# Kernel optimization log

Hardware: AMD Instinct MI355X
Metric: run time of the kernel (lower is better)

Reference implementation:

```python
import jax, jax.numpy as jnp
import numpy as np

HEADS = 4


def rel_to_abs(x):
    """Convert relative logits [..., L, 2L-1] to absolute [..., L, L].
    out[..., i, j] = x[..., i, j - i + L - 1]."""
    L = x.shape[-2]
    idx = jnp.arange(L)[None, :] - jnp.arange(L)[:, None] + (L - 1)  # [L, L]
    idx = jnp.broadcast_to(idx, x.shape[:-1] + (L,))
    return jnp.take_along_axis(x, idx, axis=-1)


def setup_inputs() -> dict:
    key = jax.random.key(0)
    ks = jax.random.split(key, 5)
    b, c, h, w = 2, 256, 64, 64
    dh = c // HEADS
    return {
        "x": jax.random.normal(ks[0], (b, c, h, w), jnp.float32),
        "w_qkv": jax.random.normal(ks[1], (3 * c, c), jnp.float32) / np.float32(np.sqrt(c)),
        "w_out": jax.random.normal(ks[2], (c, c), jnp.float32) / np.float32(np.sqrt(c)),
        "rel_height": jax.random.normal(ks[3], (2 * h - 1, dh), jnp.float32),
        "rel_width": jax.random.normal(ks[4], (2 * w - 1, dh), jnp.float32),
    }


def reference(x, w_qkv, w_out, rel_height, rel_width):
    b, c, h, w = x.shape
    dh = c // HEADS
    N = h * w
    scale = dh ** -0.5

    # 1x1 conv == per-pixel matmul over channels
    qkv = jnp.einsum('bchw,oc->bohw', x, w_qkv)  # [b, 3c, h, w]
    q, k, v = jnp.split(qkv, 3, axis=1)

    def to_heads(t):  # [b, c, h, w] -> [b, H, N, dh]
        return t.reshape(b, HEADS, dh, N).transpose(0, 1, 3, 2)

    q = to_heads(q) * scale
    k = to_heads(k)
    v = to_heads(v)

    # content-content scores over spatial positions
    content = jnp.einsum('bnid,bnjd->bnij', q, k)  # [b, H, N, N]

    q5 = q.reshape(b, HEADS, h, w, dh)  # [b, H, x, y, dh]
    # width relative logits: [b,H,x,y,2w-1] -> abs -> [b,H,x,y,jw]
    rw = rel_to_abs(jnp.einsum('bnxyd,rd->bnxyr', q5, rel_width))
    # height relative logits on transposed spatial: [b,H,y,x,2h-1] -> [b,H,y,x,jh]
    rh = rel_to_abs(jnp.einsum('bnyxd,rd->bnyxr', q5.transpose(0, 1, 3, 2, 4), rel_height))

    logits = content.reshape(b, HEADS, h, w, h, w)
    logits = logits + rw[:, :, :, :, None, :]  # broadcast width bias over target height jh
    logits = logits + rh.transpose(0, 1, 3, 2, 4)[:, :, :, :, :, None]  # [b,H,x,y,jh] over jw

    attn = jax.nn.softmax(logits.reshape(b, HEADS, N, N), axis=-1)
    out = jnp.einsum('bnij,bnjd->bnid', attn, v)  # [b, H, N, dh]
    out = out.transpose(0, 1, 3, 2).reshape(b, c, h, w)
    out = jnp.einsum('bchw,oc->bohw', out, w_out)  # 1x1 out projection
    return out + x
```

## Files before the change

kernel.cpp:

```cpp
#include <hip/hip_runtime.h>

typedef unsigned short u16;
typedef unsigned int u32;
typedef __bf16 bf16x8 __attribute__((ext_vector_type(8)));
typedef __bf16 bf16x2 __attribute__((ext_vector_type(2)));
typedef float f32x4 __attribute__((ext_vector_type(4)));
typedef float f32x2 __attribute__((ext_vector_type(2)));
typedef u32 u32x4 __attribute__((ext_vector_type(4)));
typedef u32 u32x2 __attribute__((ext_vector_type(2)));
typedef short s16x4 __attribute__((ext_vector_type(4)));

#define DEVI __device__ __forceinline__

#if defined(__has_builtin)
#if __has_builtin(__builtin_amdgcn_exp2f)
#define EXP2F(x) __builtin_amdgcn_exp2f(x)
#endif
#endif
#ifndef EXP2F
#define EXP2F(x) exp2f(x)
#endif

#define MFMA16(a, b, c) __builtin_amdgcn_mfma_f32_16x16x32_bf16(a, b, c, 0, 0, 0)
#define MFMA1K(a, b, c) __builtin_amdgcn_mfma_f32_16x16x16bf16_1k(a, b, c, 0, 0, 0)

DEVI u16 f2bf(float f) {
    u32 u = __builtin_bit_cast(u32, f);
    u = (u + 0x7FFFu + ((u >> 16) & 1u)) >> 16;
    return (u16)u;
}
DEVI float bf2f(u16 h) {
    u32 u = ((u32)h) << 16;
    return __builtin_bit_cast(float, u);
}
DEVI float bfhi(u32 u) { return __builtin_bit_cast(float, u & 0xFFFF0000u); }
DEVI float bflo(u32 u) { return __builtin_bit_cast(float, u << 16); }
DEVI bf16x8 bc8(u32x4 u) { return __builtin_bit_cast(bf16x8, u); }
DEVI u32 pack2(float a, float b) {
    f32x2 v = {a, b};
    bf16x2 h = __builtin_convertvector(v, bf16x2);
    return __builtin_bit_cast(u32, h);
}

#define QSCALE 0.18033688011112042f

__global__ __launch_bounds__(256) void k_prep(const float* __restrict__ x,
                                              const float* __restrict__ wq,
                                              const float* __restrict__ wo,
                                              const float* __restrict__ relh,
                                              const float* __restrict__ relw,
                                              u16* __restrict__ xt, u16* __restrict__ wqb,
                                              u16* __restrict__ wob, u16* __restrict__ relhb,
                                              u16* __restrict__ relwb) {
    int bid = blockIdx.x;
    int t = threadIdx.x;
    if (bid < 512) {
        int pm = bid & 63, cm = (bid >> 6) & 3, b = bid >> 8;
        int p0 = pm * 64, c0 = cm * 64;
        __shared__ float tile[64][65];
#pragma unroll
        for (int it = 0; it < 16; ++it) {
            int idx = it * 256 + t;
            int cl = idx >> 6, pl = idx & 63;
            tile[cl][pl] = x[((size_t)(b * 256 + c0 + cl)) * 4096 + p0 + pl];
        }
        __syncthreads();
#pragma unroll
        for (int it = 0; it < 16; ++it) {
            int idx = it * 256 + t;
            int pl = idx >> 6, cl = idx & 63;
            xt[((size_t)(b * 4096 + p0 + pl)) * 256 + c0 + cl] = f2bf(tile[cl][pl]);
        }
    } else {
        int i0 = (bid - 512) * 256 + t;
#pragma unroll
        for (int i = i0; i < 196608; i += 65536) wqb[i] = f2bf(wq[i]);
        if (i0 < 65536) wob[i0] = f2bf(wo[i0]);
        if (i0 < 8192) {
            relhb[i0] = (i0 < 8128) ? f2bf(relh[i0]) : (u16)0;
            relwb[i0] = (i0 < 8128) ? f2bf(relw[i0]) : (u16)0;
        }
    }
}

__global__ __launch_bounds__(256) void k_qkv(const u16* __restrict__ xt, const u16* __restrict__ wqb,
                                             const u16* __restrict__ relwb,
                                             const u16* __restrict__ relhb,
                                             u16* __restrict__ q, u16* __restrict__ k,
                                             u16* __restrict__ vt, u16* __restrict__ Wabs,
                                             u16* __restrict__ Habs) {
    int pm = blockIdx.x, on = blockIdx.y, b = blockIdx.z;
    int p0 = pm * 64, o0 = on * 64;
    __shared__ __align__(16) u16 Bt[64 * 264];
    int t = threadIdx.x;
    int wv = t >> 6, l = t & 63, quad = l >> 4, li = l & 15;

    u32x4 areg[8];
    const u32x4* arow = (const u32x4*)(xt + ((size_t)(b * 4096 + p0 + wv * 16 + li)) * 256);
#pragma unroll
    for (int kc = 0; kc < 8; ++kc) areg[kc] = arow[kc * 4 + quad];

    {
        int row = t >> 2, c0 = (t & 3) * 64;
        const u32x4* g = (const u32x4*)(wqb + (size_t)(o0 + row) * 256 + c0);
        u32x4* s = (u32x4*)(Bt + row * 264 + c0);
#pragma unroll
        for (int kk = 0; kk < 8; ++kk) s[kk] = g[kk];
    }
    __syncthreads();

    f32x4 acc[4] = {{0, 0, 0, 0}, {0, 0, 0, 0}, {0, 0, 0, 0}, {0, 0, 0, 0}};
#pragma unroll
    for (int kc = 0; kc < 8; ++kc) {
        bf16x8 a = bc8(areg[kc]);
#pragma unroll
        for (int ct = 0; ct < 4; ++ct) {
            bf16x8 bb = bc8(*(const u32x4*)(Bt + (ct * 16 + li) * 264 + kc * 32 + quad * 8));
            acc[ct] = MFMA16(a, bb, acc[ct]);
        }
    }

    int tensor = on >> 2, head = on & 3;
    if (tensor == 2) {
        __syncthreads();
        u16* T = Bt;
#pragma unroll
        for (int ct = 0; ct < 4; ++ct)
#pragma unroll
            for (int r = 0; r < 4; ++r)
                T[(ct * 16 + li) * 72 + wv * 16 + quad * 4 + r] = f2bf(acc[ct][r]);
        __syncthreads();
        int dr = t >> 2, pc = (t & 3) * 16;
        u32x4* g = (u32x4*)(vt + ((size_t)((b * 4 + head) * 64 + dr)) * 4096 + p0 + pc);
        const u32x4* s2 = (const u32x4*)(T + dr * 72 + pc);
        g[0] = s2[0];
        g[1] = s2[1];
    } else {
        u16* outp = (tensor == 0) ? q : k;
        float sc = (tensor == 0) ? QSCALE : 1.0f;
#pragma unroll
        for (int ct = 0; ct < 4; ++ct)
#pragma unroll
            for (int r = 0; r < 4; ++r) {
                int p = p0 + wv * 16 + quad * 4 + r;
                int d = ct * 16 + li;
                outp[((size_t)((b * 4 + head) * 4096 + p)) * 64 + d] = f2bf(acc[ct][r] * sc);
            }
        if (tensor == 0) {
            int bh = b * 4 + head;
            u16* T = Bt;
            u16* Ls = Bt + 64 * 72;
            __syncthreads();
#pragma unroll
            for (int ct = 0; ct < 4; ++ct)
#pragma unroll
                for (int r = 0; r < 4; ++r)
                    T[(wv * 16 + quad * 4 + r) * 72 + ct * 16 + li] = f2bf(acc[ct][r] * QSCALE);
            {
                int row = t >> 1, half = t & 1;
                const u32x4* g2 = (const u32x4*)(relwb + row * 64 + half * 32);
                u32x4* s2 = (u32x4*)(Ls + row * 72 + half * 32);
#pragma unroll
                for (int kk = 0; kk < 4; ++kk) s2[kk] = g2[kk];
            }
            __syncthreads();
            u32x4 aq2[2];
            aq2[0] = *(const u32x4*)(T + (wv * 16 + li) * 72 + quad * 8);
            aq2[1] = *(const u32x4*)(T + (wv * 16 + li) * 72 + 32 + quad * 8);

            f32x4 acc2[8];
#pragma unroll
            for (int ct = 0; ct < 8; ++ct) acc2[ct] = (f32x4){0.f, 0.f, 0.f, 0.f};
#pragma unroll
            for (int kc = 0; kc < 2; ++kc) {
                bf16x8 a = bc8(aq2[kc]);
#pragma unroll
                for (int ct = 0; ct < 8; ++ct) {
                    bf16x8 bb = bc8(*(const u32x4*)(Ls + (ct * 16 + li) * 72 + kc * 32 + quad * 8));
                    acc2[ct] = MFMA16(a, bb, acc2[ct]);
                }
            }
#pragma unroll
            for (int ct = 0; ct < 8; ++ct)
#pragma unroll
                for (int r = 0; r < 4; ++r) {
                    int row = wv * 16 + quad * 4 + r;
                    int j = (ct * 16 + li) - 63 + row;
                    if (j >= 0 && j < 64)
                        Wabs[((size_t)(bh * 4096 + p0 + row)) * 64 + j] = f2bf(acc2[ct][r]);
                }
            __syncthreads();
            {
                int row = t >> 1, half = t & 1;
                const u32x4* g2 = (const u32x4*)(relhb + row * 64 + half * 32);
                u32x4* s2 = (u32x4*)(Ls + row * 72 + half * 32);
#pragma unroll
                for (int kk = 0; kk < 4; ++kk) s2[kk] = g2[kk];
            }
            __syncthreads();
#pragma unroll
            for (int ct = 0; ct < 8; ++ct) acc2[ct] = (f32x4){0.f, 0.f, 0.f, 0.f};
#pragma unroll
            for (int kc = 0; kc < 2; ++kc) {
                bf16x8 a = bc8(aq2[kc]);
#pragma unroll
                for (int ct = 0; ct < 8; ++ct) {
                    bf16x8 bb = bc8(*(const u32x4*)(Ls + (ct * 16 + li) * 72 + kc * 32 + quad * 8));
                    acc2[ct] = MFMA16(a, bb, acc2[ct]);
                }
            }
#pragma unroll
            for (int ct = 0; ct < 8; ++ct)
#pragma unroll
                for (int r = 0; r < 4; ++r) {
                    int row = wv * 16 + quad * 4 + r;
                    int j = (ct * 16 + li) - 63 + pm;
                    if (j >= 0 && j < 64)
                        Habs[((size_t)(bh * 4096 + p0 + row)) * 64 + j] = f2bf(acc2[ct][r]);
                }
        }
    }
}

__global__ __launch_bounds__(256, 2) void k_flash(const u16* __restrict__ q,
                                                  const u16* __restrict__ kg,
                                                  const u16* __restrict__ vt,
                                                  const u16* __restrict__ Wabs,
                                                  const u16* __restrict__ Habs,
                                                  u16* __restrict__ OP,
                                                  float* __restrict__ LS) {
    int pm = blockIdx.x, bh = blockIdx.y, ks = blockIdx.z;
    int p0 = pm * 128;
    __shared__ __align__(16) u16 Kt[2][64 * 72];
    __shared__ __align__(16) u16 Vl[2][64 * 72];
    __shared__ __align__(16) u16 Hl[128 * 24];
    int t = threadIdx.x, wv = t >> 6, l = t & 63, quad = l >> 4, li = l & 15;
    int rbase = wv * 32;

    u32x4 aq[2][2];
#pragma unroll
    for (int rs = 0; rs < 2; ++rs) {
        const u32x4* qrow =
            (const u32x4*)(q + ((size_t)(bh * 4096 + p0 + rbase + rs * 16 + li)) * 64);
        aq[rs][0] = qrow[quad];
        aq[rs][1] = qrow[4 + quad];
    }

    f32x4 wb4[2][4];
#pragma unroll
    for (int rs = 0; rs < 2; ++rs)
#pragma unroll
        for (int ct = 0; ct < 4; ++ct) {
            const u32* wp = (const u32*)(Wabs +
                                         ((size_t)(bh * 4096 + p0 + rbase + rs * 16 + li)) * 64 +
                                         ct * 16 + quad * 4);
            u32 lo = wp[0], hi = wp[1];
            wb4[rs][ct] = (f32x4){bflo(lo), bfhi(lo), bflo(hi), bfhi(hi)};
        }

    {
        int row = t >> 1, half = t & 1;
        const u32x4* g =
            (const u32x4*)(Habs + ((size_t)(bh * 4096 + p0 + row)) * 64 + ks * 16 + half * 8);
        *(u32x4*)(Hl + row * 24 + half * 8) = g[0];
    }

    int srow = t >> 2, scc = (t & 3) * 16;
    {
        int j0 = ks * 1024;
        const u32x4* gk = (const u32x4*)(kg + ((size_t)(bh * 4096 + j0 + srow)) * 64 + scc);
        u32x4* sk = (u32x4*)(Kt[0] + srow * 72 + scc);
        sk[0] = gk[0];
        sk[1] = gk[1];
        const u32x4* gv = (const u32x4*)(vt + ((size_t)(bh * 64 + srow)) * 4096 + j0 + scc);
        u32x4* sv = (u32x4*)(Vl[0] + srow * 72 + scc);
        sv[0] = gv[0];
        sv[1] = gv[1];
    }

    f32x4 oacc[2][5];
#pragma unroll
    for (int rs = 0; rs < 2; ++rs)
#pragma unroll
        for (int ct = 0; ct < 5; ++ct) oacc[rs][ct] = (f32x4){0.f, 0.f, 0.f, 0.f};

    const s16x4 ones = {(short)0x3F80, (short)0x3F80, (short)0x3F80, (short)0x3F80};

    u32x4 kreg[2], vreg[2];
    for (int kt = 0; kt < 16; ++kt) {
        __syncthreads();
        int cur = kt & 1;
        const u16* Kc = Kt[cur];
        const u16* Vc = Vl[cur];
        if (kt < 15) {
            int j0 = (ks * 16 + kt + 1) * 64;
            const u32x4* gk = (const u32x4*)(kg + ((size_t)(bh * 4096 + j0 + srow)) * 64 + scc);
            kreg[0] = gk[0];
            kreg[1] = gk[1];
            const u32x4* gv = (const u32x4*)(vt + ((size_t)(bh * 64 + srow)) * 4096 + j0 + scc);
            vreg[0] = gv[0];
            vreg[1] = gv[1];
        }

        float hh0 = bf2f(Hl[(rbase + li) * 24 + kt]);
        float hh1 = bf2f(Hl[(rbase + 16 + li) * 24 + kt]);
        f32x4 s[2][4];
#pragma unroll
        for (int ct = 0; ct < 4; ++ct) {
            s[0][ct] = wb4[0][ct] + hh0;
            s[1][ct] = wb4[1][ct] + hh1;
        }
#pragma unroll
        for (int kc = 0; kc < 2; ++kc) {
            bf16x8 b0 = bc8(aq[0][kc]), b1 = bc8(aq[1][kc]);
#pragma unroll
            for (int ct = 0; ct < 4; ++ct) {
                bf16x8 af = bc8(*(const u32x4*)(Kc + (ct * 16 + li) * 72 + kc * 32 + quad * 8));
                s[0][ct] = MFMA16(af, b0, s[0][ct]);
                s[1][ct] = MFMA16(af, b1, s[1][ct]);
            }
        }

        s16x4 pf[2][4];
#pragma unroll
        for (int rs = 0; rs < 2; ++rs)
#pragma unroll
            for (int ct = 0; ct < 4; ++ct) {
                u32x2 pp;
                pp.x = pack2(EXP2F(s[rs][ct][0]), EXP2F(s[rs][ct][1]));
                pp.y = pack2(EXP2F(s[rs][ct][2]), EXP2F(s[rs][ct][3]));
                pf[rs][ct] = __builtin_bit_cast(s16x4, pp);
            }

#pragma unroll
        for (int jt = 0; jt < 4; ++jt) {
            s16x4 a0 = pf[0][jt], a1 = pf[1][jt];
#pragma unroll
            for (int dt = 0; dt < 4; ++dt) {
                s16x4 bv = __builtin_bit_cast(
                    s16x4, *(const u32x2*)(Vc + (dt * 16 + li) * 72 + jt * 16 + quad * 4));
                oacc[0][dt] = MFMA1K(a0, bv, oacc[0][dt]);
                oacc[1][dt] = MFMA1K(a1, bv, oacc[1][dt]);
            }
            oacc[0][4] = MFMA1K(a0, ones, oacc[0][4]);
            oacc[1][4] = MFMA1K(a1, ones, oacc[1][4]);
        }

        if (kt < 15) {
            u32x4* sk = (u32x4*)(Kt[cur ^ 1] + srow * 72 + scc);
            sk[0] = kreg[0];
            sk[1] = kreg[1];
            u32x4* sv = (u32x4*)(Vl[cur ^ 1] + srow * 72 + scc);
            sv[0] = vreg[0];
            sv[1] = vreg[1];
        }
    }

#pragma unroll
    for (int rs = 0; rs < 2; ++rs) {
#pragma unroll
        for (int ct = 0; ct < 4; ++ct)
#pragma unroll
            for (int r = 0; r < 4; ++r) {
                int p = p0 + rbase + rs * 16 + quad * 4 + r;
                OP[((size_t)((ks * 8 + bh) * 4096 + p)) * 64 + ct * 16 + li] =
                    f2bf(oacc[rs][ct][r]);
            }
        if (li == 0) {
#pragma unroll
            for (int r = 0; r < 4; ++r) {
                int p = p0 + rbase + rs * 16 + quad * 4 + r;
                LS[(size_t)(ks * 8 + bh) * 4096 + p] = oacc[rs][4][r];
            }
        }
    }
}

__global__ __launch_bounds__(256) void k_out2(const u16* __restrict__ wob,
                                              const u16* __restrict__ OP,
                                              const float* __restrict__ LS,
                                              const float* __restrict__ x,
                                              float* __restrict__ out) {
    int pm = blockIdx.x, b = blockIdx.y, com = blockIdx.z;
    int p0 = pm * 64;
    __shared__ __align__(16) u16 Bt[64 * 264];
    int t = threadIdx.x, wv = t >> 6, l = t & 63, quad = l >> 4, li = l & 15;

    {
        int row = t >> 2, head = t & 3;
        int bh = b * 4 + head;
        int p = p0 + row;
        const u32x4* op[4];
        float lsum = 0.f;
#pragma unroll
        for (int s2 = 0; s2 < 4; ++s2) {
            op[s2] = (const u32x4*)(OP + ((size_t)((s2 * 8 + bh) * 4096 + p)) * 64);
            lsum += LS[(size_t)(s2 * 8 + bh) * 4096 + p];
        }
        float linv = 1.0f / lsum;
        u16* dst = Bt + row * 264 + head * 64;
#pragma unroll
        for (int kk = 0; kk < 8; ++kk) {
            u32x4 a = op[0][kk], c = op[1][kk], e = op[2][kk], f = op[3][kk];
            u32x4 pk;
            pk.x = pack2((bflo(a.x) + bflo(c.x) + bflo(e.x) + bflo(f.x)) * linv,
                         (bfhi(a.x) + bfhi(c.x) + bfhi(e.x) + bfhi(f.x)) * linv);
            pk.y = pack2((bflo(a.y) + bflo(c.y) + bflo(e.y) + bflo(f.y)) * linv,
                         (bfhi(a.y) + bfhi(c.y) + bfhi(e.y) + bfhi(f.y)) * linv);
            pk.z = pack2((bflo(a.z) + bflo(c.z) + bflo(e.z) + bflo(f.z)) * linv,
                         (bfhi(a.z) + bfhi(c.z) + bfhi(e.z) + bfhi(f.z)) * linv);
            pk.w = pack2((bflo(a.w) + bflo(c.w) + bflo(e.w) + bflo(f.w)) * linv,
                         (bfhi(a.w) + bfhi(c.w) + bfhi(e.w) + bfhi(f.w)) * linv);
            *(u32x4*)(dst + kk * 8) = pk;
        }
    }
    __syncthreads();

    int co0 = com * 64;
    f32x4 acc[4] = {{0, 0, 0, 0}, {0, 0, 0, 0}, {0, 0, 0, 0}, {0, 0, 0, 0}};
    const u32x4* arow = (const u32x4*)(wob + (size_t)(co0 + wv * 16 + li) * 256);
#pragma unroll
    for (int kc = 0; kc < 8; ++kc) {
        bf16x8 a = bc8(arow[kc * 4 + quad]);
#pragma unroll
        for (int ct = 0; ct < 4; ++ct) {
            bf16x8 bb = bc8(*(const u32x4*)(Bt + (ct * 16 + li) * 264 + kc * 32 + quad * 8));
            acc[ct] = MFMA16(a, bb, acc[ct]);
        }
    }
#pragma unroll
    for (int ct = 0; ct < 4; ++ct)
#pragma unroll
        for (int r = 0; r < 4; ++r) {
            size_t idx =
                ((size_t)(b * 256 + co0 + wv * 16 + quad * 4 + r)) * 4096 + p0 + ct * 16 + li;
            out[idx] = acc[ct][r] + x[idx];
        }
}

extern "C" void kernel_launch(void* const* d_in, const int* in_sizes, int n_in, void* d_out,
                              int out_size, void* d_ws, size_t ws_size, hipStream_t stream) {
    const float* x = (const float*)d_in[0];
    const float* wqkv = (const float*)d_in[1];
    const float* wout = (const float*)d_in[2];
    const float* relh = (const float*)d_in[3];
    const float* relw = (const float*)d_in[4];
    float* out = (float*)d_out;
    char* ws = (char*)d_ws;

    u16* xt = (u16*)(ws + 0);
    u16* wqb = (u16*)(ws + 4194304);
    u16* wob = (u16*)(ws + 4587520);
    u16* relwb = (u16*)(ws + 4718592);
    u16* relhb = (u16*)(ws + 4734976);
    u16* qb = (u16*)(ws + 4751360);
    u16* kb = (u16*)(ws + 8945664);
    u16* vtb = (u16*)(ws + 13139968);
    u16* Wabs = (u16*)(ws + 17334272);
    u16* Habs = (u16*)(ws + 21528576);
    u16* OPart = (u16*)(ws + 25722880);
    float* LSum = (float*)(ws + 0);

    k_prep<<<768, 256, 0, stream>>>(x, wqkv, wout, relh, relw, xt, wqb, wob, relhb, relwb);
    k_qkv<<<dim3(64, 12, 2), 256, 0, stream>>>(xt, wqb, relwb, relhb, qb, kb, vtb, Wabs, Habs);
    k_flash<<<dim3(32, 8, 4), 256, 0, stream>>>(qb, kb, vtb, Wabs, Habs, OPart, LSum);
    k_out2<<<dim3(64, 2, 4), 256, 0, stream>>>(wob, OPart, LSum, x, out);
}
```

Measured before the change: 153.6 us.

## Use direct global-to-LDS loads with XOR swizzle and halve flash key split

Replaces register-staged K/V and weight tile copies with global_load_lds direct-to-LDS transfers, using an XOR-rotated layout in place of padded rows to avoid bank conflicts. The flash kernel's key split drops from 4 to 2 chunks, so each block loops over 32 tiles instead of 16, and the output kernel merges 2 partials and computes two output channel tiles per block. This cuts VGPR staging and partial-merge traffic but halves flash grid parallelism and adds a full vmcnt wait before every barrier.

```diff
diff --git a/kernel.cpp b/kernel.cpp
--- a/kernel.cpp
+++ b/kernel.cpp
@@ -23,6 +23,13 @@
 
 #define MFMA16(a, b, c) __builtin_amdgcn_mfma_f32_16x16x32_bf16(a, b, c, 0, 0, 0)
 #define MFMA1K(a, b, c) __builtin_amdgcn_mfma_f32_16x16x16bf16_1k(a, b, c, 0, 0, 0)
+
+typedef __attribute__((address_space(1))) u32 gu32;
+typedef __attribute__((address_space(3))) u32 lu32;
+DEVI void gll16(const u16* g, u16* l) {
+    __builtin_amdgcn_global_load_lds((const gu32*)g, (lu32*)l, 16, 0, 0);
+}
+#define WAIT_VM0() __builtin_amdgcn_s_waitcnt(0x0f70)
 
 DEVI u16 f2bf(float f) {
     u32 u = __builtin_bit_cast(u32, f);
@@ -91,7 +98,7 @@
                                              u16* __restrict__ Habs) {
     int pm = blockIdx.x, on = blockIdx.y, b = blockIdx.z;
     int p0 = pm * 64, o0 = on * 64;
-    __shared__ __align__(16) u16 Bt[64 * 264];
+    __shared__ __align__(16) u16 Sm[64 * 256];
     int t = threadIdx.x;
     int wv = t >> 6, l = t & 63, quad = l >> 4, li = l & 15;
 
@@ -101,12 +108,15 @@
     for (int kc = 0; kc < 8; ++kc) areg[kc] = arow[kc * 4 + quad];
 
     {
-        int row = t >> 2, c0 = (t & 3) * 64;
-        const u32x4* g = (const u32x4*)(wqb + (size_t)(o0 + row) * 256 + c0);
-        u32x4* s = (u32x4*)(Bt + row * 264 + c0);
-#pragma unroll
-        for (int kk = 0; kk < 8; ++kk) s[kk] = g[kk];
-    }
+        int pc = l & 31;
+#pragma unroll
+        for (int i = 0; i < 8; ++i) {
+            int r = wv * 16 + i * 2 + (l >> 5);
+            gll16(wqb + (size_t)(o0 + r) * 256 + ((pc + r) & 31) * 8,
+                  Sm + (wv * 16 + i * 2) * 256);
+        }
+    }
+    WAIT_VM0();
     __syncthreads();
 
     f32x4 acc[4] = {{0, 0, 0, 0}, {0, 0, 0, 0}, {0, 0, 0, 0}, {0, 0, 0, 0}};
@@ -115,7 +125,8 @@
         bf16x8 a = bc8(areg[kc]);
 #pragma unroll
         for (int ct = 0; ct < 4; ++ct) {
-            bf16x8 bb = bc8(*(const u32x4*)(Bt + (ct * 16 + li) * 264 + kc * 32 + quad * 8));
+            bf16x8 bb = bc8(*(const u32x4*)(Sm + (ct * 16 + li) * 256 +
+                                            (((kc * 4 + quad) - (ct * 16 + li)) & 31) * 8));
             acc[ct] = MFMA16(a, bb, acc[ct]);
         }
     }
@@ -123,7 +134,7 @@
     int tensor = on >> 2, head = on & 3;
     if (tensor == 2) {
         __syncthreads();
-        u16* T = Bt;
+        u16* T = Sm;
 #pragma unroll
         for (int ct = 0; ct < 4; ++ct)
 #pragma unroll
@@ -148,8 +159,8 @@
             }
         if (tensor == 0) {
             int bh = b * 4 + head;
-            u16* T = Bt;
-            u16* Ls = Bt + 64 * 72;
+            u16* T = Sm;
+            u16* Ls = Sm + 64 * 72;
             __syncthreads();
 #pragma unroll
             for (int ct = 0; ct < 4; ++ct)
@@ -231,9 +242,9 @@
                                                   float* __restrict__ LS) {
     int pm = blockIdx.x, bh = blockIdx.y, ks = blockIdx.z;
     int p0 = pm * 128;
-    __shared__ __align__(16) u16 Kt[2][64 * 72];
-    __shared__ __align__(16) u16 Vl[2][64 * 72];
-    __shared__ __align__(16) u16 Hl[128 * 24];
+    __shared__ __align__(16) u16 Kt[2][64 * 64];
+    __shared__ __align__(16) u16 Vl[2][64 * 64];
+    __shared__ __align__(16) u16 Hl[128 * 40];
     int t = threadIdx.x, wv = t >> 6, l = t & 63, quad = l >> 4, li = l & 15;
     int rbase = wv * 32;
 
@@ -261,21 +272,24 @@
     {
         int row = t >> 1, half = t & 1;
         const u32x4* g =
-            (const u32x4*)(Habs + ((size_t)(bh * 4096 + p0 + row)) * 64 + ks * 16 + half * 8);
-        *(u32x4*)(Hl + row * 24 + half * 8) = g[0];
-    }
-
-    int srow = t >> 2, scc = (t & 3) * 16;
+            (const u32x4*)(Habs + ((size_t)(bh * 4096 + p0 + row)) * 64 + ks * 32 + half * 16);
+        *(u32x4*)(Hl + row * 40 + half * 16) = g[0];
+        *(u32x4*)(Hl + row * 40 + half * 16 + 8) = g[1];
+    }
+
+    int grow = wv * 16 + (l >> 3);
+    int gchk = l & 7;
+
     {
-        int j0 = ks * 1024;
-        const u32x4* gk = (const u32x4*)(kg + ((size_t)(bh * 4096 + j0 + srow)) * 64 + scc);
-        u32x4* sk = (u32x4*)(Kt[0] + srow * 72 + scc);
-        sk[0] = gk[0];
-        sk[1] = gk[1];
-        const u32x4* gv = (const u32x4*)(vt + ((size_t)(bh * 64 + srow)) * 4096 + j0 + scc);
-        u32x4* sv = (u32x4*)(Vl[0] + srow * 72 + scc);
-        sv[0] = gv[0];
-        sv[1] = gv[1];
+        int j0 = ks * 2048;
+#pragma unroll
+        for (int i = 0; i < 2; ++i) {
+            int r = grow + i * 8;
+            gll16(kg + ((size_t)(bh * 4096 + j0 + r)) * 64 + ((gchk + r) & 7) * 8,
+                  (u16*)Kt[0] + (wv * 16 + i * 8) * 64);
+            gll16(vt + ((size_t)(bh * 64 + r)) * 4096 + j0 + ((gchk + r) & 7) * 8,
+                  (u16*)Vl[0] + (wv * 16 + i * 8) * 64);
+        }
     }
 
     f32x4 oacc[2][5];
@@ -286,24 +300,26 @@
 
     const s16x4 ones = {(short)0x3F80, (short)0x3F80, (short)0x3F80, (short)0x3F80};
 
-    u32x4 kreg[2], vreg[2];
-    for (int kt = 0; kt < 16; ++kt) {
+    for (int kt = 0; kt < 32; ++kt) {
+        WAIT_VM0();
         __syncthreads();
         int cur = kt & 1;
-        const u16* Kc = Kt[cur];
-        const u16* Vc = Vl[cur];
-        if (kt < 15) {
-            int j0 = (ks * 16 + kt + 1) * 64;
-            const u32x4* gk = (const u32x4*)(kg + ((size_t)(bh * 4096 + j0 + srow)) * 64 + scc);
-            kreg[0] = gk[0];
-            kreg[1] = gk[1];
-            const u32x4* gv = (const u32x4*)(vt + ((size_t)(bh * 64 + srow)) * 4096 + j0 + scc);
-            vreg[0] = gv[0];
-            vreg[1] = gv[1];
-        }
-
-        float hh0 = bf2f(Hl[(rbase + li) * 24 + kt]);
-        float hh1 = bf2f(Hl[(rbase + 16 + li) * 24 + kt]);
+        const u16* Kc = (const u16*)Kt[cur];
+        const u16* Vc = (const u16*)Vl[cur];
+        if (kt < 31) {
+            int j0 = (ks * 32 + kt + 1) * 64;
+#pragma unroll
+            for (int i = 0; i < 2; ++i) {
+                int r = grow + i * 8;
+                gll16(kg + ((size_t)(bh * 4096 + j0 + r)) * 64 + ((gchk + r) & 7) * 8,
+                      (u16*)Kt[cur ^ 1] + (wv * 16 + i * 8) * 64);
+                gll16(vt + ((size_t)(bh * 64 + r)) * 4096 + j0 + ((gchk + r) & 7) * 8,
+                      (u16*)Vl[cur ^ 1] + (wv * 16 + i * 8) * 64);
+            }
+        }
+
+        float hh0 = bf2f(Hl[(rbase + li) * 40 + kt]);
+        float hh1 = bf2f(Hl[(rbase + 16 + li) * 40 + kt]);
         f32x4 s[2][4];
 #pragma unroll
         for (int ct = 0; ct < 4; ++ct) {
@@ -315,7 +331,8 @@
             bf16x8 b0 = bc8(aq[0][kc]), b1 = bc8(aq[1][kc]);
 #pragma unroll
             for (int ct = 0; ct < 4; ++ct) {
-                bf16x8 af = bc8(*(const u32x4*)(Kc + (ct * 16 + li) * 72 + kc * 32 + quad * 8));
+                bf16x8 af = bc8(*(const u32x4*)(Kc + (ct * 16 + li) * 64 +
+                                                (((kc * 4 + quad) - li) & 7) * 8));
                 s[0][ct] = MFMA16(af, b0, s[0][ct]);
                 s[1][ct] = MFMA16(af, b1, s[1][ct]);
             }
@@ -338,21 +355,14 @@
 #pragma unroll
             for (int dt = 0; dt < 4; ++dt) {
                 s16x4 bv = __builtin_bit_cast(
-                    s16x4, *(const u32x2*)(Vc + (dt * 16 + li) * 72 + jt * 16 + quad * 4));
+                    s16x4, *(const u32x2*)(Vc + (dt * 16 + li) * 64 +
+                                           (((2 * jt + (quad >> 1)) - li) & 7) * 8 +
+                                           (quad & 1) * 4));
                 oacc[0][dt] = MFMA1K(a0, bv, oacc[0][dt]);
                 oacc[1][dt] = MFMA1K(a1, bv, oacc[1][dt]);
             }
             oacc[0][4] = MFMA1K(a0, ones, oacc[0][4]);
             oacc[1][4] = MFMA1K(a1, ones, oacc[1][4]);
-        }
-
-        if (kt < 15) {
-            u32x4* sk = (u32x4*)(Kt[cur ^ 1] + srow * 72 + scc);
-            sk[0] = kreg[0];
-            sk[1] = kreg[1];
-            u32x4* sv = (u32x4*)(Vl[cur ^ 1] + srow * 72 + scc);
-            sv[0] = vreg[0];
-            sv[1] = vreg[1];
         }
     }
 
@@ -381,7 +391,7 @@
                                               const float* __restrict__ LS,
                                               const float* __restrict__ x,
                                               float* __restrict__ out) {
-    int pm = blockIdx.x, b = blockIdx.y, com = blockIdx.z;
+    int pm = blockIdx.x, b = blockIdx.y, coh = blockIdx.z;
     int p0 = pm * 64;
     __shared__ __align__(16) u16 Bt[64 * 264];
     int t = threadIdx.x, wv = t >> 6, l = t & 63, quad = l >> 4, li = l & 15;
@@ -390,52 +400,47 @@
         int row = t >> 2, head = t & 3;
         int bh = b * 4 + head;
         int p = p0 + row;
-        const u32x4* op[4];
-        float lsum = 0.f;
-#pragma unroll
-        for (int s2 = 0; s2 < 4; ++s2) {
-            op[s2] = (const u32x4*)(OP + ((size_t)((s2 * 8 + bh) * 4096 + p)) * 64);
-            lsum += LS[(size_t)(s2 * 8 + bh) * 4096 + p];
-        }
-        float linv = 1.0f / lsum;
+        const u32x4* o0p = (const u32x4*)(OP + ((size_t)(bh * 4096 + p)) * 64);
+        const u32x4* o1p = (const u32x4*)(OP + ((size_t)((8 + bh) * 4096 + p)) * 64);
+        float linv = 1.0f / (LS[(size_t)bh * 4096 + p] + LS[(size_t)(8 + bh) * 4096 + p]);
         u16* dst = Bt + row * 264 + head * 64;
 #pragma unroll
         for (int kk = 0; kk < 8; ++kk) {
-            u32x4 a = op[0][kk], c = op[1][kk], e = op[2][kk], f = op[3][kk];
+            u32x4 a = o0p[kk], c = o1p[kk];
             u32x4 pk;
-            pk.x = pack2((bflo(a.x) + bflo(c.x) + bflo(e.x) + bflo(f.x)) * linv,
-                         (bfhi(a.x) + bfhi(c.x) + bfhi(e.x) + bfhi(f.x)) * linv);
-            pk.y = pack2((bflo(a.y) + bflo(c.y) + bflo(e.y) + bflo(f.y)) * linv,
-                         (bfhi(a.y) + bfhi(c.y) + bfhi(e.y) + bfhi(f.y)) * linv);
-            pk.z = pack2((bflo(a.z) + bflo(c.z) + bflo(e.z) + bflo(f.z)) * linv,
-                         (bfhi(a.z) + bfhi(c.z) + bfhi(e.z) + bfhi(f.z)) * linv);
-            pk.w = pack2((bflo(a.w) + bflo(c.w) + bflo(e.w) + bflo(f.w)) * linv,
-                         (bfhi(a.w) + bfhi(c.w) + bfhi(e.w) + bfhi(f.w)) * linv);
+            pk.x = pack2((bflo(a.x) + bflo(c.x)) * linv, (bfhi(a.x) + bfhi(c.x)) * linv);
+            pk.y = pack2((bflo(a.y) + bflo(c.y)) * linv, (bfhi(a.y) + bfhi(c.y)) * linv);
+            pk.z = pack2((bflo(a.z) + bflo(c.z)) * linv, (bfhi(a.z) + bfhi(c.z)) * linv);
+            pk.w = pack2((bflo(a.w) + bflo(c.w)) * linv, (bfhi(a.w) + bfhi(c.w)) * linv);
             *(u32x4*)(dst + kk * 8) = pk;
         }
     }
     __syncthreads();
 
-    int co0 = com * 64;
-    f32x4 acc[4] = {{0, 0, 0, 0}, {0, 0, 0, 0}, {0, 0, 0, 0}, {0, 0, 0, 0}};
-    const u32x4* arow = (const u32x4*)(wob + (size_t)(co0 + wv * 16 + li) * 256);
-#pragma unroll
-    for (int kc = 0; kc < 8; ++kc) {
-        bf16x8 a = bc8(arow[kc * 4 + quad]);
-#pragma unroll
-        for (int ct = 0; ct < 4; ++ct) {
-            bf16x8 bb = bc8(*(const u32x4*)(Bt + (ct * 16 + li) * 264 + kc * 32 + quad * 8));
-            acc[ct] = MFMA16(a, bb, acc[ct]);
-        }
-    }
-#pragma unroll
-    for (int ct = 0; ct < 4; ++ct)
-#pragma unroll
-        for (int r = 0; r < 4; ++r) {
-            size_t idx =
-                ((size_t)(b * 256 + co0 + wv * 16 + quad * 4 + r)) * 4096 + p0 + ct * 16 + li;
-            out[idx] = acc[ct][r] + x[idx];
-        }
+#pragma unroll
+    for (int ci = 0; ci < 2; ++ci) {
+        int com = coh * 2 + ci;
+        int co0 = com * 64;
+        f32x4 acc[4] = {{0, 0, 0, 0}, {0, 0, 0, 0}, {0, 0, 0, 0}, {0, 0, 0, 0}};
+        const u32x4* arow = (const u32x4*)(wob + (size_t)(co0 + wv * 16 + li) * 256);
+#pragma unroll
+        for (int kc = 0; kc < 8; ++kc) {
+            bf16x8 a = bc8(arow[kc * 4 + quad]);
+#pragma unroll
+            for (int ct = 0; ct < 4; ++ct) {
+                bf16x8 bb = bc8(*(const u32x4*)(Bt + (ct * 16 + li) * 264 + kc * 32 + quad * 8));
+                acc[ct] = MFMA16(a, bb, acc[ct]);
+            }
+        }
+#pragma unroll
+        for (int ct = 0; ct < 4; ++ct)
+#pragma unroll
+            for (int r = 0; r < 4; ++r) {
+                size_t idx =
+                    ((size_t)(b * 256 + co0 + wv * 16 + quad * 4 + r)) * 4096 + p0 + ct * 16 + li;
+                out[idx] = acc[ct][r] + x[idx];
+            }
+    }
 }
 
 extern "C" void kernel_launch(void* const* d_in, const int* in_sizes, int n_in, void* d_out,
@@ -463,6 +468,6 @@
 
     k_prep<<<768, 256, 0, stream>>>(x, wqkv, wout, relh, relw, xt, wqb, wob, relhb, relwb);
     k_qkv<<<dim3(64, 12, 2), 256, 0, stream>>>(xt, wqb, relwb, relhb, qb, kb, vtb, Wabs, Habs);
-    k_flash<<<dim3(32, 8, 4), 256, 0, stream>>>(qb, kb, vtb, Wabs, Habs, OPart, LSum);
-    k_out2<<<dim3(64, 2, 4), 256, 0, stream>>>(wob, OPart, LSum, x, out);
-}
+    k_flash<<<dim3(32, 8, 2), 256, 0, stream>>>(qb, kb, vtb, Wabs, Habs, OPart, LSum);
+    k_out2<<<dim3(64, 2, 2), 256, 0, stream>>>(wob, OPart, LSum, x, out);
+}
```

Result: slower. 157.1 us (+2.3%).
